# Optimization experiments

Measured on AMD Instinct MI355X. Metric: run time of the kernel, lower is better.

Reference implementation:

```python
import jax, jax.numpy as jnp
import numpy as np

HEADS = 16
D_MODEL = 1024
D_K = D_MODEL // HEADS
SEQ = 2048
BSZ = 2


def softmax_one(x, axis):
    # softmax with an extra +1 in the denominator ("attention off" slot)
    x = x - jnp.max(x, axis=axis, keepdims=True)
    ex = jnp.exp(x)
    return ex / (1.0 + jnp.sum(ex, axis=axis, keepdims=True))


def setup_inputs() -> dict:
    key = jax.random.key(0)
    ks = jax.random.split(key, 7)
    s = 1.0 / np.sqrt(D_MODEL)
    return {
        "x": jax.random.normal(ks[0], (SEQ, BSZ, D_MODEL), dtype=jnp.float32),
        "Wq": jax.random.normal(ks[1], (D_MODEL, D_MODEL), dtype=jnp.float32) * s,
        "bq": jnp.zeros((D_MODEL,), dtype=jnp.float32),
        "Wk": jax.random.normal(ks[2], (D_MODEL, D_MODEL), dtype=jnp.float32) * s,
        "bk": jnp.zeros((D_MODEL,), dtype=jnp.float32),
        "Wv": jax.random.normal(ks[3], (D_MODEL, D_MODEL), dtype=jnp.float32) * s,
        "bv": jnp.zeros((D_MODEL,), dtype=jnp.float32),
    }


def reference(x, Wq, bq, Wk, bk, Wv, bv):
    S, B, D = x.shape
    q = (x @ Wq.T + bq).reshape(S, B, HEADS, D_K)
    k = (x @ Wk.T + bk).reshape(S, B, HEADS, D_K)
    v = (x @ Wv.T + bv).reshape(S, B, HEADS, D_K)
    # [i, j, b, h] full score tensor, scaled by sqrt(d_k)
    scores = jnp.einsum('ibhd,jbhd->ijbh', q, k) / np.sqrt(D_K).astype(np.float32)
    causal = jnp.tril(jnp.ones((S, S), dtype=bool))[:, :, None, None]
    scores = jnp.where(causal, scores, -jnp.inf)
    attn = softmax_one(scores, axis=1)  # softmax over key axis j with +1 denom
    out = jnp.einsum('ijbh,jbhd->ibhd', attn, v)
    return out.reshape(S, B, D)
```

## Files before the change

### kernel.cpp

```cpp
#include <hip/hip_runtime.h>

#define SEQ 2048
#define BSZ 2
#define NH 16
#define DKD 64
#define DM 1024
#define NROW (SEQ*BSZ)
#define KDIM 1024

typedef __attribute__((ext_vector_type(8))) short bf16x8;
typedef __attribute__((ext_vector_type(4))) float floatx4;

__device__ __forceinline__ unsigned short f2b(float f) {
  unsigned int u = __builtin_bit_cast(unsigned int, f);
  u += 0x7fffu + ((u >> 16) & 1u);
  return (unsigned short)(u >> 16);
}

__device__ __forceinline__ void async_copy16(void* lds, const void* g) {
  __builtin_amdgcn_global_load_lds(
      (__attribute__((address_space(1))) void*)(void*)g,
      (__attribute__((address_space(3))) void*)lds, 16, 0, 0);
}

__device__ __forceinline__ floatx4 mfma16(bf16x8 a, bf16x8 b, floatx4 c) {
  return __builtin_amdgcn_mfma_f32_16x16x32_bf16(a, b, c, 0, 0, 0);
}

__global__ __launch_bounds__(256) void cvt_kernel(
    const float* __restrict__ x, const float* __restrict__ Wq,
    const float* __restrict__ Wk, const float* __restrict__ Wv,
    ushort* __restrict__ xbf, ushort* __restrict__ wbf) {
  size_t tid = (size_t)blockIdx.x * 256 + threadIdx.x;
  size_t i4 = tid * 4;
  const float* src;
  const size_t NX = (size_t)NROW * KDIM;
  ushort* dst;
  size_t off;
  if (i4 < NX) {
    src = x; off = i4; dst = xbf + i4;
  } else {
    size_t wix = i4 - NX;
    int proj = (int)(wix >> 20);
    src = proj == 0 ? Wq : (proj == 1 ? Wk : Wv);
    off = wix & 1048575u;
    dst = wbf + wix;
  }
  float4 v = *(const float4*)(src + off);
  ushort4 o;
  o.x = f2b(v.x); o.y = f2b(v.y); o.z = f2b(v.z); o.w = f2b(v.w);
  *(ushort4*)dst = o;
}

__global__ __launch_bounds__(256, 2) void gemm_qkv(
    const ushort* __restrict__ xbf, const ushort* __restrict__ wbf,
    const float* __restrict__ bq, const float* __restrict__ bk,
    const float* __restrict__ bvv,
    ushort* __restrict__ Qs, ushort* __restrict__ Ks, ushort* __restrict__ Vt) {
  __shared__ ushort Al[128 * 32];
  __shared__ ushort Bl[128 * 32];
  __shared__ ushort Cl[128 * 136];
  const int t = threadIdx.x;
  const int w = t >> 6, l = t & 63;
  const int wr = w >> 1, wc = w & 1;
  const int lane15 = l & 15, quad = l >> 4;
  const int rb = blockIdx.x, cb = blockIdx.y;
  const ushort* Ag = xbf + (size_t)rb * 128 * KDIM;
  const ushort* Bg = wbf + (size_t)cb * 128 * KDIM;
  const int rsub = l >> 2, c2 = (l & 3) * 8;

  floatx4 acc[4][4];
  #pragma unroll
  for (int i = 0; i < 4; ++i)
    #pragma unroll
    for (int j = 0; j < 4; ++j) acc[i][j] = (floatx4){0.f, 0.f, 0.f, 0.f};

  for (int kk = 0; kk < KDIM; kk += 32) {
    __syncthreads();
    #pragma unroll
    for (int half = 0; half < 2; ++half) {
      int rloc = w * 32 + half * 16;
      async_copy16(&Al[rloc * 32], Ag + (size_t)(rloc + rsub) * KDIM + kk + c2);
      async_copy16(&Bl[rloc * 32], Bg + (size_t)(rloc + rsub) * KDIM + kk + c2);
    }
    __syncthreads();
    bf16x8 af[4], bfr[4];
    #pragma unroll
    for (int mt = 0; mt < 4; ++mt)
      af[mt] = *(const bf16x8*)&Al[(wr * 64 + mt * 16 + lane15) * 32 + quad * 8];
    #pragma unroll
    for (int nt = 0; nt < 4; ++nt)
      bfr[nt] = *(const bf16x8*)&Bl[(wc * 64 + nt * 16 + lane15) * 32 + quad * 8];
    #pragma unroll
    for (int mt = 0; mt < 4; ++mt)
      #pragma unroll
      for (int nt = 0; nt < 4; ++nt)
        acc[mt][nt] = mfma16(af[mt], bfr[nt], acc[mt][nt]);
  }

  int proj = (cb * 128) >> 10;
  const float* bias = proj == 0 ? bq : (proj == 1 ? bk : bvv);
  float scale = proj == 0 ? 0.125f * 1.44269504088896f : 1.0f;
  bool isV = (proj == 2);

  #pragma unroll
  for (int nt = 0; nt < 4; ++nt) {
    int c = wc * 64 + nt * 16 + lane15;
    int cip = (cb * 128 + c) & 1023;
    float bias_v = bias[cip];
    #pragma unroll
    for (int mt = 0; mt < 4; ++mt) {
      #pragma unroll
      for (int r = 0; r < 4; ++r) {
        int n = wr * 64 + mt * 16 + quad * 4 + r;
        float val = (acc[mt][nt][r] + bias_v) * scale;
        if (!isV) Cl[n * 136 + c] = f2b(val);
        else      Cl[c * 136 + (n & 1) * 64 + (n >> 1)] = f2b(val);
      }
    }
  }
  __syncthreads();

  if (!isV) {
    ushort* dst = proj == 0 ? Qs : Ks;
    int b = t >> 7;
    int sl = t & 63;
    int chunk = (t >> 6) & 1;
    int n = (sl << 1) | b;
    int cip = (cb * 128 + chunk * 64) & 1023;
    int h = cip >> 6;
    int s = rb * 64 + sl;
    ushort* g = dst + (((size_t)(b * NH + h) * SEQ + s) * DKD);
    const uint4* s4 = (const uint4*)&Cl[n * 136 + chunk * 64];
    #pragma unroll
    for (int j = 0; j < 8; ++j) *(uint4*)(g + j * 8) = s4[j];
  } else {
    int c = t >> 1, b = t & 1;
    int cip = (cb * 128 + c) & 1023;
    int h = cip >> 6, dk = c & 63;
    ushort* g = Vt + ((size_t)(b * NH + h) * DKD + dk) * SEQ + rb * 64;
    const uint4* s4 = (const uint4*)&Cl[c * 136 + b * 64];
    #pragma unroll
    for (int j = 0; j < 8; ++j) *(uint4*)(g + j * 8) = s4[j];
  }
}

__global__ __launch_bounds__(256, 2) void attn_kernel(
    const ushort* __restrict__ Qs, const ushort* __restrict__ Ks,
    const ushort* __restrict__ Vt, float* __restrict__ out) {
  __shared__ ushort Kl[2][64 * 72];
  __shared__ ushort Vl[2][64 * 72];
  __shared__ ushort Pl[4][16 * 72];
  const int t = threadIdx.x;
  const int w = t >> 6, l = t & 63;
  const int lane15 = l & 15, quad = l >> 4;
  const int qa = blockIdx.x;
  const int bh = blockIdx.y;
  const int b = bh >> 4, h = bh & 15;
  const int qtB = 31 - qa;

  const ushort* Kg = Ks + (size_t)bh * SEQ * DKD;
  const ushort* Vg = Vt + (size_t)bh * DKD * SEQ;
  const int srow = t >> 3;
  const int scol = (t & 7) * 8;

  int qt = qa;
  int qbase = qt * 64;
  const ushort* Qg = Qs + ((size_t)bh * SEQ + qbase + w * 16 + lane15) * DKD;
  bf16x8 qf0 = *(const bf16x8*)(Qg + quad * 8);
  bf16x8 qf1 = *(const bf16x8*)(Qg + 32 + quad * 8);

  floatx4 o[4];
  #pragma unroll
  for (int i = 0; i < 4; ++i) o[i] = (floatx4){0.f, 0.f, 0.f, 0.f};
  floatx4 lacc = (floatx4){0.f, 0.f, 0.f, 0.f};
  float m_r[4] = {-1e30f, -1e30f, -1e30f, -1e30f};

  bf16x8 ones;
  #pragma unroll
  for (int j = 0; j < 8; ++j) ones[j] = (short)0x3F80;

  #define KT_OF(j) ((j) <= qa ? (j) : (j) - qa - 1)

  uint4 kr0, kr1, vr0, vr1;
  {
    int kt0 = 0;
    kr0 = *(const uint4*)(Kg + (size_t)(kt0 * 64 + srow) * DKD + scol);
    kr1 = *(const uint4*)(Kg + (size_t)(kt0 * 64 + srow + 32) * DKD + scol);
    vr0 = *(const uint4*)(Vg + (size_t)srow * SEQ + kt0 * 64 + scol);
    vr1 = *(const uint4*)(Vg + (size_t)(srow + 32) * SEQ + kt0 * 64 + scol);
    *(uint4*)&Kl[0][srow * 72 + scol] = kr0;
    *(uint4*)&Kl[0][(srow + 32) * 72 + scol] = kr1;
    *(uint4*)&Vl[0][srow * 72 + scol] = vr0;
    *(uint4*)&Vl[0][(srow + 32) * 72 + scol] = vr1;
    int kt1 = KT_OF(1);
    kr0 = *(const uint4*)(Kg + (size_t)(kt1 * 64 + srow) * DKD + scol);
    kr1 = *(const uint4*)(Kg + (size_t)(kt1 * 64 + srow + 32) * DKD + scol);
    vr0 = *(const uint4*)(Vg + (size_t)srow * SEQ + kt1 * 64 + scol);
    vr1 = *(const uint4*)(Vg + (size_t)(srow + 32) * SEQ + kt1 * 64 + scol);
  }

  for (int it = 0; it <= 32; ++it) {
    const int cur = it & 1;
    const int kt = KT_OF(it);
    __syncthreads();

    floatx4 sf[4];
    #pragma unroll
    for (int nt = 0; nt < 4; ++nt) {
      floatx4 a = (floatx4){0.f, 0.f, 0.f, 0.f};
      bf16x8 k0 = *(const bf16x8*)&Kl[cur][(nt * 16 + lane15) * 72 + quad * 8];
      bf16x8 k1 = *(const bf16x8*)&Kl[cur][(nt * 16 + lane15) * 72 + 32 + quad * 8];
      a = mfma16(qf0, k0, a);
      a = mfma16(qf1, k1, a);
      sf[nt] = a;
    }

    if (kt == qt) {
      #pragma unroll
      for (int nt = 0; nt < 4; ++nt) {
        int j = kt * 64 + nt * 16 + lane15;
        #pragma unroll
        for (int r = 0; r < 4; ++r) {
          int i = qbase + w * 16 + quad * 4 + r;
          if (j > i) sf[nt][r] = -1e30f;
        }
      }
    }

    float alpha[4];
    #pragma unroll
    for (int r = 0; r < 4; ++r) {
      float v = fmaxf(fmaxf(sf[0][r], sf[1][r]), fmaxf(sf[2][r], sf[3][r]));
      v = fmaxf(v, __shfl_xor(v, 1, 64));
      v = fmaxf(v, __shfl_xor(v, 2, 64));
      v = fmaxf(v, __shfl_xor(v, 4, 64));
      v = fmaxf(v, __shfl_xor(v, 8, 64));
      float mn = fmaxf(m_r[r], v);
      alpha[r] = __builtin_amdgcn_exp2f(m_r[r] - mn);
      m_r[r] = mn;
    }
    ushort* Pw = &Pl[w][0];
    #pragma unroll
    for (int nt = 0; nt < 4; ++nt)
      #pragma unroll
      for (int r = 0; r < 4; ++r) {
        float p = __builtin_amdgcn_exp2f(sf[nt][r] - m_r[r]);
        Pw[(quad * 4 + r) * 72 + nt * 16 + lane15] =
            (ushort)(__builtin_bit_cast(unsigned int, p) >> 16);
      }
    #pragma unroll
    for (int ntd = 0; ntd < 4; ++ntd)
      #pragma unroll
      for (int r = 0; r < 4; ++r) o[ntd][r] *= alpha[r];
    #pragma unroll
    for (int r = 0; r < 4; ++r) lacc[r] *= alpha[r];

    asm volatile("s_waitcnt lgkmcnt(0)" ::: "memory");
    bf16x8 pa0 = *(const bf16x8*)&Pw[lane15 * 72 + quad * 8];
    bf16x8 pa1 = *(const bf16x8*)&Pw[lane15 * 72 + 32 + quad * 8];

    lacc = mfma16(pa0, ones, lacc);
    lacc = mfma16(pa1, ones, lacc);

    #pragma unroll
    for (int ntd = 0; ntd < 4; ++ntd) {
      bf16x8 v0 = *(const bf16x8*)&Vl[cur][(ntd * 16 + lane15) * 72 + quad * 8];
      bf16x8 v1 = *(const bf16x8*)&Vl[cur][(ntd * 16 + lane15) * 72 + 32 + quad * 8];
      o[ntd] = mfma16(pa0, v0, o[ntd]);
      o[ntd] = mfma16(pa1, v1, o[ntd]);
    }

    if (it == qa || it == 32) {
      float inv[4];
      #pragma unroll
      for (int r = 0; r < 4; ++r) inv[r] = 1.0f / (1.0f + lacc[r]);
      #pragma unroll
      for (int ntd = 0; ntd < 4; ++ntd) {
        int d = h * DKD + ntd * 16 + lane15;
        #pragma unroll
        for (int r = 0; r < 4; ++r) {
          int i = qbase + w * 16 + quad * 4 + r;
          out[((size_t)i * BSZ + b) * DM + d] = o[ntd][r] * inv[r];
        }
      }
      if (it == qa) {
        #pragma unroll
        for (int i = 0; i < 4; ++i) o[i] = (floatx4){0.f, 0.f, 0.f, 0.f};
        lacc = (floatx4){0.f, 0.f, 0.f, 0.f};
        #pragma unroll
        for (int r = 0; r < 4; ++r) m_r[r] = -1e30f;
        qt = qtB;
        qbase = qt * 64;
        const ushort* Qg2 = Qs + ((size_t)bh * SEQ + qbase + w * 16 + lane15) * DKD;
        qf0 = *(const bf16x8*)(Qg2 + quad * 8);
        qf1 = *(const bf16x8*)(Qg2 + 32 + quad * 8);
      }
    }

    if (it < 32) {
      int nxt = cur ^ 1;
      *(uint4*)&Kl[nxt][srow * 72 + scol] = kr0;
      *(uint4*)&Kl[nxt][(srow + 32) * 72 + scol] = kr1;
      *(uint4*)&Vl[nxt][srow * 72 + scol] = vr0;
      *(uint4*)&Vl[nxt][(srow + 32) * 72 + scol] = vr1;
      if (it + 2 <= 32) {
        int kt2 = KT_OF(it + 2);
        kr0 = *(const uint4*)(Kg + (size_t)(kt2 * 64 + srow) * DKD + scol);
        kr1 = *(const uint4*)(Kg + (size_t)(kt2 * 64 + srow + 32) * DKD + scol);
        vr0 = *(const uint4*)(Vg + (size_t)srow * SEQ + kt2 * 64 + scol);
        vr1 = *(const uint4*)(Vg + (size_t)(srow + 32) * SEQ + kt2 * 64 + scol);
      }
    }
  }
  #undef KT_OF
}

extern "C" void kernel_launch(void* const* d_in, const int* in_sizes, int n_in,
                              void* d_out, int out_size, void* d_ws, size_t ws_size,
                              hipStream_t stream) {
  (void)in_sizes; (void)n_in; (void)out_size; (void)ws_size;
  const float* x  = (const float*)d_in[0];
  const float* Wq = (const float*)d_in[1];
  const float* bq = (const float*)d_in[2];
  const float* Wk = (const float*)d_in[3];
  const float* bk = (const float*)d_in[4];
  const float* Wv = (const float*)d_in[5];
  const float* bv = (const float*)d_in[6];
  float* out = (float*)d_out;

  ushort* xbf = (ushort*)d_out;
  ushort* wbf = (ushort*)((char*)d_out + 8388608);

  char* ws = (char*)d_ws;
  ushort* Qs = (ushort*)(ws);
  ushort* Ks = (ushort*)(ws + 8388608);
  ushort* Vt = (ushort*)(ws + 16777216);

  cvt_kernel<<<dim3(7168), dim3(256), 0, stream>>>(x, Wq, Wk, Wv, xbf, wbf);
  gemm_qkv<<<dim3(32, 24), dim3(256), 0, stream>>>(xbf, wbf, bq, bk, bv, Qs, Ks, Vt);
  attn_kernel<<<dim3(16, 32), dim3(256), 0, stream>>>(Qs, Ks, Vt, out);
}
```

Measured before the change: 174.8 us.

## Drop online-softmax rescaling and LDS staging; load K/V fragments directly to registers

Result: slower. 268.6 us (+53.7%).

```diff
diff --git a/kernel.cpp b/kernel.cpp
--- a/kernel.cpp
+++ b/kernel.cpp
@@ -7,6 +7,7 @@
 #define DM 1024
 #define NROW (SEQ*BSZ)
 #define KDIM 1024
+#define BIAS 16.0f
 
 typedef __attribute__((ext_vector_type(8))) short bf16x8;
 typedef __attribute__((ext_vector_type(4))) float floatx4;
@@ -148,21 +149,18 @@
 __global__ __launch_bounds__(256, 2) void attn_kernel(
     const ushort* __restrict__ Qs, const ushort* __restrict__ Ks,
     const ushort* __restrict__ Vt, float* __restrict__ out) {
-  __shared__ ushort Kl[2][64 * 72];
-  __shared__ ushort Vl[2][64 * 72];
   __shared__ ushort Pl[4][16 * 72];
   const int t = threadIdx.x;
   const int w = t >> 6, l = t & 63;
   const int lane15 = l & 15, quad = l >> 4;
-  const int qa = blockIdx.x;
-  const int bh = blockIdx.y;
+  const int bh = blockIdx.x;
+  const int qa = blockIdx.y;
   const int b = bh >> 4, h = bh & 15;
-  const int qtB = 31 - qa;
 
   const ushort* Kg = Ks + (size_t)bh * SEQ * DKD;
   const ushort* Vg = Vt + (size_t)bh * DKD * SEQ;
-  const int srow = t >> 3;
-  const int scol = (t & 7) * 8;
+  const ushort* kp0 = Kg + (size_t)lane15 * DKD + quad * 8;
+  const ushort* vp0 = Vg + (size_t)lane15 * SEQ + quad * 8;
 
   int qt = qa;
   int qbase = qt * 64;
@@ -174,145 +172,124 @@
   #pragma unroll
   for (int i = 0; i < 4; ++i) o[i] = (floatx4){0.f, 0.f, 0.f, 0.f};
   floatx4 lacc = (floatx4){0.f, 0.f, 0.f, 0.f};
-  float m_r[4] = {-1e30f, -1e30f, -1e30f, -1e30f};
+  float pmax[4] = {-1e30f, -1e30f, -1e30f, -1e30f};
 
   bf16x8 ones;
   #pragma unroll
   for (int j = 0; j < 8; ++j) ones[j] = (short)0x3F80;
 
+  ushort* Pw = &Pl[w][0];
+
   #define KT_OF(j) ((j) <= qa ? (j) : (j) - qa - 1)
 
-  uint4 kr0, kr1, vr0, vr1;
-  {
-    int kt0 = 0;
-    kr0 = *(const uint4*)(Kg + (size_t)(kt0 * 64 + srow) * DKD + scol);
-    kr1 = *(const uint4*)(Kg + (size_t)(kt0 * 64 + srow + 32) * DKD + scol);
-    vr0 = *(const uint4*)(Vg + (size_t)srow * SEQ + kt0 * 64 + scol);
-    vr1 = *(const uint4*)(Vg + (size_t)(srow + 32) * SEQ + kt0 * 64 + scol);
-    *(uint4*)&Kl[0][srow * 72 + scol] = kr0;
-    *(uint4*)&Kl[0][(srow + 32) * 72 + scol] = kr1;
-    *(uint4*)&Vl[0][srow * 72 + scol] = vr0;
-    *(uint4*)&Vl[0][(srow + 32) * 72 + scol] = vr1;
-    int kt1 = KT_OF(1);
-    kr0 = *(const uint4*)(Kg + (size_t)(kt1 * 64 + srow) * DKD + scol);
-    kr1 = *(const uint4*)(Kg + (size_t)(kt1 * 64 + srow + 32) * DKD + scol);
-    vr0 = *(const uint4*)(Vg + (size_t)srow * SEQ + kt1 * 64 + scol);
-    vr1 = *(const uint4*)(Vg + (size_t)(srow + 32) * SEQ + kt1 * 64 + scol);
-  }
-
-  for (int it = 0; it <= 32; ++it) {
-    const int cur = it & 1;
-    const int kt = KT_OF(it);
-    __syncthreads();
-
-    floatx4 sf[4];
-    #pragma unroll
-    for (int nt = 0; nt < 4; ++nt) {
-      floatx4 a = (floatx4){0.f, 0.f, 0.f, 0.f};
-      bf16x8 k0 = *(const bf16x8*)&Kl[cur][(nt * 16 + lane15) * 72 + quad * 8];
-      bf16x8 k1 = *(const bf16x8*)&Kl[cur][(nt * 16 + lane15) * 72 + 32 + quad * 8];
-      a = mfma16(qf0, k0, a);
-      a = mfma16(qf1, k1, a);
-      sf[nt] = a;
+  #define LOAD_TILE(KF, VF, KT) do {                                        \
+    const ushort* kp_ = kp0 + (size_t)(KT) * 64 * DKD;                      \
+    const ushort* vp_ = vp0 + (KT) * 64;                                    \
+    _Pragma("unroll")                                                       \
+    for (int nt = 0; nt < 4; ++nt) {                                        \
+      KF[2*nt]   = *(const bf16x8*)(kp_ + nt * 16 * DKD);                   \
+      KF[2*nt+1] = *(const bf16x8*)(kp_ + nt * 16 * DKD + 32);              \
+      VF[2*nt]   = *(const bf16x8*)(vp_ + (size_t)nt * 16 * SEQ);           \
+      VF[2*nt+1] = *(const bf16x8*)(vp_ + (size_t)nt * 16 * SEQ + 32);      \
+    }                                                                       \
+  } while (0)
+
+  #define TILE_BODY(KF, VF, IT) do {                                        \
+    const int kt_ = KT_OF(IT);                                              \
+    floatx4 sf[4];                                                          \
+    _Pragma("unroll")                                                       \
+    for (int nt = 0; nt < 4; ++nt) {                                        \
+      floatx4 a_ = (floatx4){-BIAS, -BIAS, -BIAS, -BIAS};                   \
+      a_ = mfma16(qf0, KF[2*nt], a_);                                       \
+      a_ = mfma16(qf1, KF[2*nt+1], a_);                                     \
+      sf[nt] = a_;                                                          \
+    }                                                                       \
+    if (kt_ == qt) {                                                        \
+      _Pragma("unroll")                                                     \
+      for (int nt = 0; nt < 4; ++nt) {                                      \
+        int j_ = kt_ * 64 + nt * 16 + lane15;                               \
+        _Pragma("unroll")                                                   \
+        for (int r = 0; r < 4; ++r) {                                       \
+          int i_ = qbase + w * 16 + quad * 4 + r;                           \
+          if (j_ > i_) sf[nt][r] = -1e30f;                                  \
+        }                                                                   \
+      }                                                                     \
+    }                                                                       \
+    _Pragma("unroll")                                                       \
+    for (int nt = 0; nt < 4; ++nt)                                          \
+      _Pragma("unroll")                                                     \
+      for (int r = 0; r < 4; ++r) {                                         \
+        pmax[r] = fmaxf(pmax[r], sf[nt][r]);                                \
+        float p_ = __builtin_amdgcn_exp2f(sf[nt][r]);                       \
+        Pw[(quad * 4 + r) * 72 + nt * 16 + lane15] =                        \
+            (ushort)(__builtin_bit_cast(unsigned int, p_) >> 16);           \
+      }                                                                     \
+    asm volatile("s_waitcnt lgkmcnt(0)" ::: "memory");                      \
+    bf16x8 pa0_ = *(const bf16x8*)&Pw[lane15 * 72 + quad * 8];              \
+    bf16x8 pa1_ = *(const bf16x8*)&Pw[lane15 * 72 + 32 + quad * 8];         \
+    lacc = mfma16(pa0_, ones, lacc);                                        \
+    lacc = mfma16(pa1_, ones, lacc);                                        \
+    _Pragma("unroll")                                                       \
+    for (int ntd = 0; ntd < 4; ++ntd) {                                     \
+      o[ntd] = mfma16(pa0_, VF[2*ntd], o[ntd]);                             \
+      o[ntd] = mfma16(pa1_, VF[2*ntd+1], o[ntd]);                           \
+    }                                                                       \
+    if ((IT) == qa || (IT) == 32) {                                         \
+      float mx_[4], inv_[4];                                                \
+      _Pragma("unroll")                                                     \
+      for (int r = 0; r < 4; ++r) {                                         \
+        float v_ = pmax[r];                                                 \
+        v_ = fmaxf(v_, __shfl_xor(v_, 1, 64));                              \
+        v_ = fmaxf(v_, __shfl_xor(v_, 2, 64));                              \
+        v_ = fmaxf(v_, __shfl_xor(v_, 4, 64));                              \
+        v_ = fmaxf(v_, __shfl_xor(v_, 8, 64));                              \
+        mx_[r] = v_;                                                        \
+        inv_[r] = 1.0f / (__builtin_amdgcn_exp2f(v_) + lacc[r]);            \
+      }                                                                     \
+      _Pragma("unroll")                                                     \
+      for (int ntd = 0; ntd < 4; ++ntd) {                                   \
+        int d_ = h * DKD + ntd * 16 + lane15;                               \
+        _Pragma("unroll")                                                   \
+        for (int r = 0; r < 4; ++r) {                                       \
+          int i_ = qbase + w * 16 + quad * 4 + r;                           \
+          out[((size_t)i_ * BSZ + b) * DM + d_] = o[ntd][r] * inv_[r];      \
+        }                                                                   \
+      }                                                                     \
+      if ((IT) == qa) {                                                     \
+        _Pragma("unroll")                                                   \
+        for (int i = 0; i < 4; ++i) o[i] = (floatx4){0.f, 0.f, 0.f, 0.f};   \
+        lacc = (floatx4){0.f, 0.f, 0.f, 0.f};                               \
+        _Pragma("unroll")                                                   \
+        for (int r = 0; r < 4; ++r) pmax[r] = -1e30f;                       \
+        qt = 31 - qa;                                                       \
+        qbase = qt * 64;                                                    \
+        const ushort* Qg2_ =                                                \
+            Qs + ((size_t)bh * SEQ + qbase + w * 16 + lane15) * DKD;        \
+        qf0 = *(const bf16x8*)(Qg2_ + quad * 8);                            \
+        qf1 = *(const bf16x8*)(Qg2_ + 32 + quad * 8);                       \
+      }                                                                     \
+      (void)mx_;                                                            \
+    }                                                                       \
+  } while (0)
+
+  bf16x8 ka[8], va[8], kb[8], vb[8];
+  LOAD_TILE(ka, va, 0);
+
+  #pragma unroll 1
+  for (int ii = 0; ii < 17; ++ii) {
+    {
+      const int it = 2 * ii;
+      if (it < 32) { const int ktn = KT_OF(it + 1); LOAD_TILE(kb, vb, ktn); }
+      TILE_BODY(ka, va, it);
     }
-
-    if (kt == qt) {
-      #pragma unroll
-      for (int nt = 0; nt < 4; ++nt) {
-        int j = kt * 64 + nt * 16 + lane15;
-        #pragma unroll
-        for (int r = 0; r < 4; ++r) {
-          int i = qbase + w * 16 + quad * 4 + r;
-          if (j > i) sf[nt][r] = -1e30f;
-        }
-      }
+    if (ii < 16) {
+      const int it = 2 * ii + 1;
+      { const int ktn = KT_OF(it + 1); LOAD_TILE(ka, va, ktn); }
+      TILE_BODY(kb, vb, it);
     }
-
-    float alpha[4];
-    #pragma unroll
-    for (int r = 0; r < 4; ++r) {
-      float v = fmaxf(fmaxf(sf[0][r], sf[1][r]), fmaxf(sf[2][r], sf[3][r]));
-      v = fmaxf(v, __shfl_xor(v, 1, 64));
-      v = fmaxf(v, __shfl_xor(v, 2, 64));
-      v = fmaxf(v, __shfl_xor(v, 4, 64));
-      v = fmaxf(v, __shfl_xor(v, 8, 64));
-      float mn = fmaxf(m_r[r], v);
-      alpha[r] = __builtin_amdgcn_exp2f(m_r[r] - mn);
-      m_r[r] = mn;
-    }
-    ushort* Pw = &Pl[w][0];
-    #pragma unroll
-    for (int nt = 0; nt < 4; ++nt)
-      #pragma unroll
-      for (int r = 0; r < 4; ++r) {
-        float p = __builtin_amdgcn_exp2f(sf[nt][r] - m_r[r]);
-        Pw[(quad * 4 + r) * 72 + nt * 16 + lane15] =
-            (ushort)(__builtin_bit_cast(unsigned int, p) >> 16);
-      }
-    #pragma unroll
-    for (int ntd = 0; ntd < 4; ++ntd)
-      #pragma unroll
-      for (int r = 0; r < 4; ++r) o[ntd][r] *= alpha[r];
-    #pragma unroll
-    for (int r = 0; r < 4; ++r) lacc[r] *= alpha[r];
-
-    asm volatile("s_waitcnt lgkmcnt(0)" ::: "memory");
-    bf16x8 pa0 = *(const bf16x8*)&Pw[lane15 * 72 + quad * 8];
-    bf16x8 pa1 = *(const bf16x8*)&Pw[lane15 * 72 + 32 + quad * 8];
-
-    lacc = mfma16(pa0, ones, lacc);
-    lacc = mfma16(pa1, ones, lacc);
-
-    #pragma unroll
-    for (int ntd = 0; ntd < 4; ++ntd) {
-      bf16x8 v0 = *(const bf16x8*)&Vl[cur][(ntd * 16 + lane15) * 72 + quad * 8];
-      bf16x8 v1 = *(const bf16x8*)&Vl[cur][(ntd * 16 + lane15) * 72 + 32 + quad * 8];
-      o[ntd] = mfma16(pa0, v0, o[ntd]);
-      o[ntd] = mfma16(pa1, v1, o[ntd]);
-    }
-
-    if (it == qa || it == 32) {
-      float inv[4];
-      #pragma unroll
-      for (int r = 0; r < 4; ++r) inv[r] = 1.0f / (1.0f + lacc[r]);
-      #pragma unroll
-      for (int ntd = 0; ntd < 4; ++ntd) {
-        int d = h * DKD + ntd * 16 + lane15;
-        #pragma unroll
-        for (int r = 0; r < 4; ++r) {
-          int i = qbase + w * 16 + quad * 4 + r;
-          out[((size_t)i * BSZ + b) * DM + d] = o[ntd][r] * inv[r];
-        }
-      }
-      if (it == qa) {
-        #pragma unroll
-        for (int i = 0; i < 4; ++i) o[i] = (floatx4){0.f, 0.f, 0.f, 0.f};
-        lacc = (floatx4){0.f, 0.f, 0.f, 0.f};
-        #pragma unroll
-        for (int r = 0; r < 4; ++r) m_r[r] = -1e30f;
-        qt = qtB;
-        qbase = qt * 64;
-        const ushort* Qg2 = Qs + ((size_t)bh * SEQ + qbase + w * 16 + lane15) * DKD;
-        qf0 = *(const bf16x8*)(Qg2 + quad * 8);
-        qf1 = *(const bf16x8*)(Qg2 + 32 + quad * 8);
-      }
-    }
-
-    if (it < 32) {
-      int nxt = cur ^ 1;
-      *(uint4*)&Kl[nxt][srow * 72 + scol] = kr0;
-      *(uint4*)&Kl[nxt][(srow + 32) * 72 + scol] = kr1;
-      *(uint4*)&Vl[nxt][srow * 72 + scol] = vr0;
-      *(uint4*)&Vl[nxt][(srow + 32) * 72 + scol] = vr1;
-      if (it + 2 <= 32) {
-        int kt2 = KT_OF(it + 2);
-        kr0 = *(const uint4*)(Kg + (size_t)(kt2 * 64 + srow) * DKD + scol);
-        kr1 = *(const uint4*)(Kg + (size_t)(kt2 * 64 + srow + 32) * DKD + scol);
-        vr0 = *(const uint4*)(Vg + (size_t)srow * SEQ + kt2 * 64 + scol);
-        vr1 = *(const uint4*)(Vg + (size_t)(srow + 32) * SEQ + kt2 * 64 + scol);
-      }
-    }
-  }
+  }
+  #undef TILE_BODY
+  #undef LOAD_TILE
   #undef KT_OF
 }
 
@@ -339,5 +316,5 @@
 
   cvt_kernel<<<dim3(7168), dim3(256), 0, stream>>>(x, Wq, Wk, Wv, xbf, wbf);
   gemm_qkv<<<dim3(32, 24), dim3(256), 0, stream>>>(xbf, wbf, bq, bk, bv, Qs, Ks, Vt);
-  attn_kernel<<<dim3(16, 32), dim3(256), 0, stream>>>(Qs, Ks, Vt, out);
-}
+  attn_kernel<<<dim3(32, 16), dim3(256), 0, stream>>>(Qs, Ks, Vt, out);
+}
```

## Replace online softmax with fixed-offset exponent and register-resident P in attention

Applied to the files above, without the earlier changes.

Result: faster. 162.8 us (-6.8%).

```diff
diff --git a/kernel.cpp b/kernel.cpp
--- a/kernel.cpp
+++ b/kernel.cpp
@@ -7,9 +7,12 @@
 #define DM 1024
 #define NROW (SEQ*BSZ)
 #define KDIM 1024
+#define BIAS 16.0f
 
 typedef __attribute__((ext_vector_type(8))) short bf16x8;
+typedef __attribute__((ext_vector_type(4))) short bf16x4;
 typedef __attribute__((ext_vector_type(4))) float floatx4;
+typedef __attribute__((ext_vector_type(2))) unsigned uint2v;
 
 __device__ __forceinline__ unsigned short f2b(float f) {
   unsigned int u = __builtin_bit_cast(unsigned int, f);
@@ -25,6 +28,17 @@
 
 __device__ __forceinline__ floatx4 mfma16(bf16x8 a, bf16x8 b, floatx4 c) {
   return __builtin_amdgcn_mfma_f32_16x16x32_bf16(a, b, c, 0, 0, 0);
+}
+
+__device__ __forceinline__ floatx4 mfma16k(bf16x4 a, bf16x4 b, floatx4 c) {
+#if __has_builtin(__builtin_amdgcn_mfma_f32_16x16x16bf16_1k)
+  return __builtin_amdgcn_mfma_f32_16x16x16bf16_1k(a, b, c, 0, 0, 0);
+#else
+  floatx4 d;
+  asm volatile("v_mfma_f32_16x16x16_bf16 %0, %1, %2, %3"
+               : "=v"(d) : "v"(a), "v"(b), "v"(c));
+  return d;
+#endif
 }
 
 __global__ __launch_bounds__(256) void cvt_kernel(
@@ -52,14 +66,17 @@
   *(ushort4*)dst = o;
 }
 
-__global__ __launch_bounds__(256, 2) void gemm_qkv(
+union GemmSmem {
+  struct { ushort Al[128 * 32]; ushort Bl[128 * 32]; } ab;
+  ushort Cl[128 * 136];
+};
+
+__global__ __launch_bounds__(256, 3) void gemm_qkv(
     const ushort* __restrict__ xbf, const ushort* __restrict__ wbf,
     const float* __restrict__ bq, const float* __restrict__ bk,
     const float* __restrict__ bvv,
     ushort* __restrict__ Qs, ushort* __restrict__ Ks, ushort* __restrict__ Vt) {
-  __shared__ ushort Al[128 * 32];
-  __shared__ ushort Bl[128 * 32];
-  __shared__ ushort Cl[128 * 136];
+  __shared__ GemmSmem sm;
   const int t = threadIdx.x;
   const int w = t >> 6, l = t & 63;
   const int wr = w >> 1, wc = w & 1;
@@ -80,23 +97,24 @@
     #pragma unroll
     for (int half = 0; half < 2; ++half) {
       int rloc = w * 32 + half * 16;
-      async_copy16(&Al[rloc * 32], Ag + (size_t)(rloc + rsub) * KDIM + kk + c2);
-      async_copy16(&Bl[rloc * 32], Bg + (size_t)(rloc + rsub) * KDIM + kk + c2);
+      async_copy16(&sm.ab.Al[rloc * 32], Ag + (size_t)(rloc + rsub) * KDIM + kk + c2);
+      async_copy16(&sm.ab.Bl[rloc * 32], Bg + (size_t)(rloc + rsub) * KDIM + kk + c2);
     }
     __syncthreads();
     bf16x8 af[4], bfr[4];
     #pragma unroll
     for (int mt = 0; mt < 4; ++mt)
-      af[mt] = *(const bf16x8*)&Al[(wr * 64 + mt * 16 + lane15) * 32 + quad * 8];
+      af[mt] = *(const bf16x8*)&sm.ab.Al[(wr * 64 + mt * 16 + lane15) * 32 + quad * 8];
     #pragma unroll
     for (int nt = 0; nt < 4; ++nt)
-      bfr[nt] = *(const bf16x8*)&Bl[(wc * 64 + nt * 16 + lane15) * 32 + quad * 8];
+      bfr[nt] = *(const bf16x8*)&sm.ab.Bl[(wc * 64 + nt * 16 + lane15) * 32 + quad * 8];
     #pragma unroll
     for (int mt = 0; mt < 4; ++mt)
       #pragma unroll
       for (int nt = 0; nt < 4; ++nt)
         acc[mt][nt] = mfma16(af[mt], bfr[nt], acc[mt][nt]);
   }
+  __syncthreads();
 
   int proj = (cb * 128) >> 10;
   const float* bias = proj == 0 ? bq : (proj == 1 ? bk : bvv);
@@ -114,8 +132,8 @@
       for (int r = 0; r < 4; ++r) {
         int n = wr * 64 + mt * 16 + quad * 4 + r;
         float val = (acc[mt][nt][r] + bias_v) * scale;
-        if (!isV) Cl[n * 136 + c] = f2b(val);
-        else      Cl[c * 136 + (n & 1) * 64 + (n >> 1)] = f2b(val);
+        if (!isV) sm.Cl[n * 136 + c] = f2b(val);
+        else      sm.Cl[c * 136 + (n & 1) * 64 + (n >> 1)] = f2b(val);
       }
     }
   }
@@ -131,7 +149,7 @@
     int h = cip >> 6;
     int s = rb * 64 + sl;
     ushort* g = dst + (((size_t)(b * NH + h) * SEQ + s) * DKD);
-    const uint4* s4 = (const uint4*)&Cl[n * 136 + chunk * 64];
+    const uint4* s4 = (const uint4*)&sm.Cl[n * 136 + chunk * 64];
     #pragma unroll
     for (int j = 0; j < 8; ++j) *(uint4*)(g + j * 8) = s4[j];
   } else {
@@ -139,7 +157,7 @@
     int cip = (cb * 128 + c) & 1023;
     int h = cip >> 6, dk = c & 63;
     ushort* g = Vt + ((size_t)(b * NH + h) * DKD + dk) * SEQ + rb * 64;
-    const uint4* s4 = (const uint4*)&Cl[c * 136 + b * 64];
+    const uint4* s4 = (const uint4*)&sm.Cl[c * 136 + b * 64];
     #pragma unroll
     for (int j = 0; j < 8; ++j) *(uint4*)(g + j * 8) = s4[j];
   }
@@ -150,14 +168,12 @@
     const ushort* __restrict__ Vt, float* __restrict__ out) {
   __shared__ ushort Kl[2][64 * 72];
   __shared__ ushort Vl[2][64 * 72];
-  __shared__ ushort Pl[4][16 * 72];
   const int t = threadIdx.x;
   const int w = t >> 6, l = t & 63;
   const int lane15 = l & 15, quad = l >> 4;
-  const int qa = blockIdx.x;
-  const int bh = blockIdx.y;
+  const int bh = blockIdx.x;
+  const int qa = blockIdx.y;
   const int b = bh >> 4, h = bh & 15;
-  const int qtB = 31 - qa;
 
   const ushort* Kg = Ks + (size_t)bh * SEQ * DKD;
   const ushort* Vg = Vt + (size_t)bh * DKD * SEQ;
@@ -174,21 +190,20 @@
   #pragma unroll
   for (int i = 0; i < 4; ++i) o[i] = (floatx4){0.f, 0.f, 0.f, 0.f};
   floatx4 lacc = (floatx4){0.f, 0.f, 0.f, 0.f};
-  float m_r[4] = {-1e30f, -1e30f, -1e30f, -1e30f};
-
-  bf16x8 ones;
+  float pm = -1e30f;
+
+  bf16x4 ones4;
   #pragma unroll
-  for (int j = 0; j < 8; ++j) ones[j] = (short)0x3F80;
+  for (int j = 0; j < 4; ++j) ones4[j] = (short)0x3F80;
 
   #define KT_OF(j) ((j) <= qa ? (j) : (j) - qa - 1)
 
   uint4 kr0, kr1, vr0, vr1;
   {
-    int kt0 = 0;
-    kr0 = *(const uint4*)(Kg + (size_t)(kt0 * 64 + srow) * DKD + scol);
-    kr1 = *(const uint4*)(Kg + (size_t)(kt0 * 64 + srow + 32) * DKD + scol);
-    vr0 = *(const uint4*)(Vg + (size_t)srow * SEQ + kt0 * 64 + scol);
-    vr1 = *(const uint4*)(Vg + (size_t)(srow + 32) * SEQ + kt0 * 64 + scol);
+    kr0 = *(const uint4*)(Kg + (size_t)srow * DKD + scol);
+    kr1 = *(const uint4*)(Kg + (size_t)(srow + 32) * DKD + scol);
+    vr0 = *(const uint4*)(Vg + (size_t)srow * SEQ + scol);
+    vr1 = *(const uint4*)(Vg + (size_t)(srow + 32) * SEQ + scol);
     *(uint4*)&Kl[0][srow * 72 + scol] = kr0;
     *(uint4*)&Kl[0][(srow + 32) * 72 + scol] = kr1;
     *(uint4*)&Vl[0][srow * 72 + scol] = vr0;
@@ -208,89 +223,81 @@
     floatx4 sf[4];
     #pragma unroll
     for (int nt = 0; nt < 4; ++nt) {
-      floatx4 a = (floatx4){0.f, 0.f, 0.f, 0.f};
+      floatx4 a = (floatx4){-BIAS, -BIAS, -BIAS, -BIAS};
       bf16x8 k0 = *(const bf16x8*)&Kl[cur][(nt * 16 + lane15) * 72 + quad * 8];
       bf16x8 k1 = *(const bf16x8*)&Kl[cur][(nt * 16 + lane15) * 72 + 32 + quad * 8];
-      a = mfma16(qf0, k0, a);
-      a = mfma16(qf1, k1, a);
+      a = mfma16(k0, qf0, a);
+      a = mfma16(k1, qf1, a);
       sf[nt] = a;
     }
 
     if (kt == qt) {
+      int q_abs = qbase + w * 16 + lane15;
       #pragma unroll
       for (int nt = 0; nt < 4; ++nt) {
-        int j = kt * 64 + nt * 16 + lane15;
         #pragma unroll
         for (int r = 0; r < 4; ++r) {
-          int i = qbase + w * 16 + quad * 4 + r;
-          if (j > i) sf[nt][r] = -1e30f;
+          int k_abs = kt * 64 + nt * 16 + quad * 4 + r;
+          if (k_abs > q_abs) sf[nt][r] = -1e30f;
         }
       }
     }
 
-    float alpha[4];
-    #pragma unroll
-    for (int r = 0; r < 4; ++r) {
-      float v = fmaxf(fmaxf(sf[0][r], sf[1][r]), fmaxf(sf[2][r], sf[3][r]));
-      v = fmaxf(v, __shfl_xor(v, 1, 64));
-      v = fmaxf(v, __shfl_xor(v, 2, 64));
-      v = fmaxf(v, __shfl_xor(v, 4, 64));
-      v = fmaxf(v, __shfl_xor(v, 8, 64));
-      float mn = fmaxf(m_r[r], v);
-      alpha[r] = __builtin_amdgcn_exp2f(m_r[r] - mn);
-      m_r[r] = mn;
-    }
-    ushort* Pw = &Pl[w][0];
-    #pragma unroll
-    for (int nt = 0; nt < 4; ++nt)
+    bf16x4 pa[4];
+    #pragma unroll
+    for (int nt = 0; nt < 4; ++nt) {
+      float p0 = __builtin_amdgcn_exp2f(sf[nt][0]);
+      float p1 = __builtin_amdgcn_exp2f(sf[nt][1]);
+      float p2 = __builtin_amdgcn_exp2f(sf[nt][2]);
+      float p3 = __builtin_amdgcn_exp2f(sf[nt][3]);
+      pm = fmaxf(pm, fmaxf(fmaxf(sf[nt][0], sf[nt][1]),
+                           fmaxf(sf[nt][2], sf[nt][3])));
+      unsigned u0 = __builtin_bit_cast(unsigned, p0);
+      unsigned u1 = __builtin_bit_cast(unsigned, p1);
+      unsigned u2 = __builtin_bit_cast(unsigned, p2);
+      unsigned u3 = __builtin_bit_cast(unsigned, p3);
+      uint2v pk;
+      pk[0] = (u0 >> 16) | (u1 & 0xffff0000u);
+      pk[1] = (u2 >> 16) | (u3 & 0xffff0000u);
+      pa[nt] = __builtin_bit_cast(bf16x4, pk);
+    }
+
+    #pragma unroll
+    for (int nt = 0; nt < 4; ++nt) lacc = mfma16k(pa[nt], ones4, lacc);
+    #pragma unroll
+    for (int ntd = 0; ntd < 4; ++ntd) {
+      #pragma unroll
+      for (int nt = 0; nt < 4; ++nt) {
+        bf16x4 vf = *(const bf16x4*)&Vl[cur][(ntd * 16 + lane15) * 72 +
+                                            nt * 16 + quad * 4];
+        o[ntd] = mfma16k(pa[nt], vf, o[ntd]);
+      }
+    }
+
+    if (it == qa || it == 32) {
+      float pmr = fmaxf(pm, __shfl_xor(pm, 16, 64));
+      pmr = fmaxf(pmr, __shfl_xor(pmr, 32, 64));
+      float inv_[4];
       #pragma unroll
       for (int r = 0; r < 4; ++r) {
-        float p = __builtin_amdgcn_exp2f(sf[nt][r] - m_r[r]);
-        Pw[(quad * 4 + r) * 72 + nt * 16 + lane15] =
-            (ushort)(__builtin_bit_cast(unsigned int, p) >> 16);
-      }
-    #pragma unroll
-    for (int ntd = 0; ntd < 4; ++ntd)
-      #pragma unroll
-      for (int r = 0; r < 4; ++r) o[ntd][r] *= alpha[r];
-    #pragma unroll
-    for (int r = 0; r < 4; ++r) lacc[r] *= alpha[r];
-
-    asm volatile("s_waitcnt lgkmcnt(0)" ::: "memory");
-    bf16x8 pa0 = *(const bf16x8*)&Pw[lane15 * 72 + quad * 8];
-    bf16x8 pa1 = *(const bf16x8*)&Pw[lane15 * 72 + 32 + quad * 8];
-
-    lacc = mfma16(pa0, ones, lacc);
-    lacc = mfma16(pa1, ones, lacc);
-
-    #pragma unroll
-    for (int ntd = 0; ntd < 4; ++ntd) {
-      bf16x8 v0 = *(const bf16x8*)&Vl[cur][(ntd * 16 + lane15) * 72 + quad * 8];
-      bf16x8 v1 = *(const bf16x8*)&Vl[cur][(ntd * 16 + lane15) * 72 + 32 + quad * 8];
-      o[ntd] = mfma16(pa0, v0, o[ntd]);
-      o[ntd] = mfma16(pa1, v1, o[ntd]);
-    }
-
-    if (it == qa || it == 32) {
-      float inv[4];
-      #pragma unroll
-      for (int r = 0; r < 4; ++r) inv[r] = 1.0f / (1.0f + lacc[r]);
+        float mq = __shfl(pmr, quad * 4 + r, 64);
+        inv_[r] = 1.0f / (__builtin_amdgcn_exp2f(mq) + lacc[r]);
+      }
       #pragma unroll
       for (int ntd = 0; ntd < 4; ++ntd) {
         int d = h * DKD + ntd * 16 + lane15;
         #pragma unroll
         for (int r = 0; r < 4; ++r) {
           int i = qbase + w * 16 + quad * 4 + r;
-          out[((size_t)i * BSZ + b) * DM + d] = o[ntd][r] * inv[r];
+          out[((size_t)i * BSZ + b) * DM + d] = o[ntd][r] * inv_[r];
         }
       }
       if (it == qa) {
         #pragma unroll
         for (int i = 0; i < 4; ++i) o[i] = (floatx4){0.f, 0.f, 0.f, 0.f};
         lacc = (floatx4){0.f, 0.f, 0.f, 0.f};
-        #pragma unroll
-        for (int r = 0; r < 4; ++r) m_r[r] = -1e30f;
-        qt = qtB;
+        pm = -1e30f;
+        qt = 31 - qa;
         qbase = qt * 64;
         const ushort* Qg2 = Qs + ((size_t)bh * SEQ + qbase + w * 16 + lane15) * DKD;
         qf0 = *(const bf16x8*)(Qg2 + quad * 8);
@@ -339,5 +346,5 @@
 
   cvt_kernel<<<dim3(7168), dim3(256), 0, stream>>>(x, Wq, Wk, Wv, xbf, wbf);
   gemm_qkv<<<dim3(32, 24), dim3(256), 0, stream>>>(xbf, wbf, bq, bk, bv, Qs, Ks, Vt);
-  attn_kernel<<<dim3(16, 32), dim3(256), 0, stream>>>(Qs, Ks, Vt, out);
-}
+  attn_kernel<<<dim3(32, 16), dim3(256), 0, stream>>>(Qs, Ks, Vt, out);
+}
```
